# Kernel optimization log

Hardware: AMD Instinct MI355X
Metric: run time of the kernel (lower is better)

The kernel has to match this reference:

```python
import jax, jax.numpy as jnp
import numpy as np

B, N, D = 4, 4096, 128

def setup_inputs() -> dict:
    key = jax.random.key(0)
    k1, k2 = jax.random.split(key)
    x = jax.random.normal(k1, (B, N, D), dtype=jnp.float32)
    a = jax.random.normal(k2, (2 * D, 1), dtype=jnp.float32)
    return {"x": x, "a": a}

def reference(x, a):
    # matmul(cat([x_i, x_j], -1), a) == x_i @ a1 + x_j @ a2, so avoid the
    # O(B*N*N*2D) concat: compute two O(B*N) projections and broadcast-add.
    a1 = a[:D, 0]   # [D]
    a2 = a[D:, 0]   # [D]
    s_i = x @ a1    # [B, N]  (row / source term)
    s_j = x @ a2    # [B, N]  (col / target term)
    e = s_i[:, :, None] + s_j[:, None, :]          # [B, N, N]
    e = jnp.where(e > 0, e, 0.2 * e)               # leaky_relu(0.2)
    attention = jax.nn.softmax(e, axis=-1)         # row softmax
    return attention[..., None]                    # [B, N, N, 1]
```

## Files before the change

### kernel.cpp

```cpp
#include <hip/hip_runtime.h>

#define BB 4
#define NN 4096
#define DD 128
#define RB 8

__global__ __launch_bounds__(256) void score_kernel(const float* __restrict__ x,
                                                    const float* __restrict__ a,
                                                    float* __restrict__ si,
                                                    float* __restrict__ sj) {
    int wave = threadIdx.x >> 6;
    int lane = threadIdx.x & 63;
    int row  = blockIdx.x * 4 + wave;
    const float* xr = x + (size_t)row * DD;
    float x0 = xr[lane];
    float x1 = xr[lane + 64];
    float d1 = x0 * a[lane]      + x1 * a[lane + 64];
    float d2 = x0 * a[DD + lane] + x1 * a[DD + lane + 64];
    #pragma unroll
    for (int off = 32; off > 0; off >>= 1) {
        d1 += __shfl_down(d1, off, 64);
        d2 += __shfl_down(d2, off, 64);
    }
    if (lane == 0) {
        si[row] = d1;
        sj[row] = d2;
    }
}

__global__ __launch_bounds__(256) void softmax_kernel(const float* __restrict__ si_g,
                                                      const float* __restrict__ sj_g,
                                                      float* __restrict__ out) {
    __shared__ float red[4];

    const int bpb  = NN / RB;
    const int b    = blockIdx.x / bpb;
    const int i0   = (blockIdx.x % bpb) * RB;
    const int wave = threadIdx.x >> 6;
    const int lane = threadIdx.x & 63;

    const float* sjb = sj_g + b * NN;
    float4 sjv[16];
    float lmax = -INFINITY;
    #pragma unroll
    for (int g = 0; g < 16; ++g) {
        sjv[g] = *reinterpret_cast<const float4*>(sjb + g * 256 + lane * 4);
        lmax = fmaxf(fmaxf(fmaxf(sjv[g].x, sjv[g].y), fmaxf(sjv[g].z, sjv[g].w)), lmax);
    }
    #pragma unroll
    for (int off = 1; off < 64; off <<= 1)
        lmax = fmaxf(lmax, __shfl_xor(lmax, off, 64));
    if (lane == 0) red[wave] = lmax;
    __syncthreads();
    const float sjmax = fmaxf(fmaxf(red[0], red[1]), fmaxf(red[2], red[3]));

    #pragma unroll
    for (int r = 0; r < RB / 4; ++r) {
        const int i = i0 + wave * (RB / 4) + r;
        const float sival = si_g[b * NN + i];
        float m = sival + sjmax;
        m = m > 0.f ? m : 0.2f * m;

        float lsum = 0.f;
        #pragma unroll
        for (int g = 0; g < 16; ++g) {
            float e0 = sival + sjv[g].x; e0 = (e0 > 0.f ? e0 : 0.2f * e0) - m;
            float e1 = sival + sjv[g].y; e1 = (e1 > 0.f ? e1 : 0.2f * e1) - m;
            float e2 = sival + sjv[g].z; e2 = (e2 > 0.f ? e2 : 0.2f * e2) - m;
            float e3 = sival + sjv[g].w; e3 = (e3 > 0.f ? e3 : 0.2f * e3) - m;
            lsum += __expf(e0) + __expf(e1) + __expf(e2) + __expf(e3);
        }
        #pragma unroll
        for (int off = 1; off < 64; off <<= 1)
            lsum += __shfl_xor(lsum, off, 64);
        const float inv = 1.f / lsum;

        float* orow = out + (size_t)(b * NN + i) * NN;
        #pragma unroll
        for (int g = 0; g < 16; ++g) {
            float e0 = sival + sjv[g].x; e0 = (e0 > 0.f ? e0 : 0.2f * e0) - m;
            float e1 = sival + sjv[g].y; e1 = (e1 > 0.f ? e1 : 0.2f * e1) - m;
            float e2 = sival + sjv[g].z; e2 = (e2 > 0.f ? e2 : 0.2f * e2) - m;
            float e3 = sival + sjv[g].w; e3 = (e3 > 0.f ? e3 : 0.2f * e3) - m;
            float4 v = make_float4(__expf(e0) * inv, __expf(e1) * inv,
                                   __expf(e2) * inv, __expf(e3) * inv);
            *reinterpret_cast<float4*>(orow + g * 256 + lane * 4) = v;
        }
    }
}

extern "C" void kernel_launch(void* const* d_in, const int* in_sizes, int n_in,
                              void* d_out, int out_size, void* d_ws, size_t ws_size,
                              hipStream_t stream) {
    const float* x = (const float*)d_in[0];
    const float* a = (const float*)d_in[1];
    float* out = (float*)d_out;
    float* si = (float*)d_ws;
    float* sj = si + BB * NN;

    score_kernel<<<(BB * NN) / 4, 256, 0, stream>>>(x, a, si, sj);
    softmax_kernel<<<(BB * NN) / RB, 256, 0, stream>>>(si, sj, out);
}
```

Before: 52.62 us.

## Factor leaky-relu softmax exponentials into per-column precomputed exp terms

The score kernel now stores exp(s_j) and exp(0.2*s_j) per column instead of s_j. The softmax kernel rebuilds each element as a per-row scale times one of the two precomputed exponentials, choosing between them by comparing against exp(-s_i). This removes every per-element transcendental from both softmax passes. In exchange it doubles the per-column register footprint (32 float4), reads twice as much column data, and risks overflow or underflow of exp(s_j) for large scores, which changes numerical behaviour.

```diff
diff --git a/kernel.cpp b/kernel.cpp
--- a/kernel.cpp
+++ b/kernel.cpp
@@ -8,7 +8,7 @@
 __global__ __launch_bounds__(256) void score_kernel(const float* __restrict__ x,
                                                     const float* __restrict__ a,
                                                     float* __restrict__ si,
-                                                    float* __restrict__ sj) {
+                                                    float2* __restrict__ e12) {
     int wave = threadIdx.x >> 6;
     int lane = threadIdx.x & 63;
     int row  = blockIdx.x * 4 + wave;
@@ -18,72 +18,81 @@
     float d1 = x0 * a[lane]      + x1 * a[lane + 64];
     float d2 = x0 * a[DD + lane] + x1 * a[DD + lane + 64];
     #pragma unroll
-    for (int off = 32; off > 0; off >>= 1) {
-        d1 += __shfl_down(d1, off, 64);
-        d2 += __shfl_down(d2, off, 64);
+    for (int off = 1; off < 64; off <<= 1) {
+        d1 += __shfl_xor(d1, off, 64);
+        d2 += __shfl_xor(d2, off, 64);
     }
     if (lane == 0) {
         si[row] = d1;
-        sj[row] = d2;
+        e12[row] = make_float2(__expf(d2), __expf(0.2f * d2));
     }
 }
 
 __global__ __launch_bounds__(256) void softmax_kernel(const float* __restrict__ si_g,
-                                                      const float* __restrict__ sj_g,
+                                                      const float2* __restrict__ e12_g,
                                                       float* __restrict__ out) {
     __shared__ float red[4];
 
-    const int bpb  = NN / RB;
-    const int b    = blockIdx.x / bpb;
-    const int i0   = (blockIdx.x % bpb) * RB;
+    const int b    = blockIdx.x >> 9;
+    const int i0   = (blockIdx.x & 511) * RB;
     const int wave = threadIdx.x >> 6;
     const int lane = threadIdx.x & 63;
 
-    const float* sjb = sj_g + b * NN;
-    float4 sjv[16];
-    float lmax = -INFINITY;
+    const float* eb = (const float*)(e12_g + b * NN);
+    float4 ev[32];
+    float emax = 0.f;
     #pragma unroll
     for (int g = 0; g < 16; ++g) {
-        sjv[g] = *reinterpret_cast<const float4*>(sjb + g * 256 + lane * 4);
-        lmax = fmaxf(fmaxf(fmaxf(sjv[g].x, sjv[g].y), fmaxf(sjv[g].z, sjv[g].w)), lmax);
+        const float* p = eb + (size_t)(g * 256 + lane * 4) * 2;
+        ev[2 * g]     = *reinterpret_cast<const float4*>(p);
+        ev[2 * g + 1] = *reinterpret_cast<const float4*>(p + 4);
+        emax = fmaxf(emax, fmaxf(ev[2 * g].x,     ev[2 * g].z));
+        emax = fmaxf(emax, fmaxf(ev[2 * g + 1].x, ev[2 * g + 1].z));
     }
     #pragma unroll
     for (int off = 1; off < 64; off <<= 1)
-        lmax = fmaxf(lmax, __shfl_xor(lmax, off, 64));
-    if (lane == 0) red[wave] = lmax;
+        emax = fmaxf(emax, __shfl_xor(emax, off, 64));
+    if (lane == 0) red[wave] = emax;
     __syncthreads();
-    const float sjmax = fmaxf(fmaxf(red[0], red[1]), fmaxf(red[2], red[3]));
+    const float Emax = fmaxf(fmaxf(red[0], red[1]), fmaxf(red[2], red[3]));
+    const float mj = __logf(Emax);
 
     #pragma unroll
     for (int r = 0; r < RB / 4; ++r) {
         const int i = i0 + wave * (RB / 4) + r;
         const float sival = si_g[b * NN + i];
-        float m = sival + sjmax;
-        m = m > 0.f ? m : 0.2f * m;
+        const float c = sival + mj;
+        const float m = c > 0.f ? c : 0.2f * c;
+        const float T  = __expf(-sival);
+        const float A1 = __expf(sival - m);
+        const float A2 = __expf(0.2f * sival - m);
 
         float lsum = 0.f;
         #pragma unroll
         for (int g = 0; g < 16; ++g) {
-            float e0 = sival + sjv[g].x; e0 = (e0 > 0.f ? e0 : 0.2f * e0) - m;
-            float e1 = sival + sjv[g].y; e1 = (e1 > 0.f ? e1 : 0.2f * e1) - m;
-            float e2 = sival + sjv[g].z; e2 = (e2 > 0.f ? e2 : 0.2f * e2) - m;
-            float e3 = sival + sjv[g].w; e3 = (e3 > 0.f ? e3 : 0.2f * e3) - m;
-            lsum += __expf(e0) + __expf(e1) + __expf(e2) + __expf(e3);
+            float4 e0 = ev[2 * g], e1 = ev[2 * g + 1];
+            float p0 = (e0.x > T) ? A1 * e0.x : A2 * e0.y;
+            float p1 = (e0.z > T) ? A1 * e0.z : A2 * e0.w;
+            float p2 = (e1.x > T) ? A1 * e1.x : A2 * e1.y;
+            float p3 = (e1.z > T) ? A1 * e1.z : A2 * e1.w;
+            lsum += (p0 + p1) + (p2 + p3);
         }
         #pragma unroll
         for (int off = 1; off < 64; off <<= 1)
             lsum += __shfl_xor(lsum, off, 64);
         const float inv = 1.f / lsum;
+        const float B1 = A1 * inv;
+        const float B2 = A2 * inv;
 
         float* orow = out + (size_t)(b * NN + i) * NN;
         #pragma unroll
         for (int g = 0; g < 16; ++g) {
-            float e0 = sival + sjv[g].x; e0 = (e0 > 0.f ? e0 : 0.2f * e0) - m;
-            float e1 = sival + sjv[g].y; e1 = (e1 > 0.f ? e1 : 0.2f * e1) - m;
-            float e2 = sival + sjv[g].z; e2 = (e2 > 0.f ? e2 : 0.2f * e2) - m;
-            float e3 = sival + sjv[g].w; e3 = (e3 > 0.f ? e3 : 0.2f * e3) - m;
-            float4 v = make_float4(__expf(e0) * inv, __expf(e1) * inv,
-                                   __expf(e2) * inv, __expf(e3) * inv);
+            float4 e0 = ev[2 * g], e1 = ev[2 * g + 1];
+            float4 v;
+            v.x = (e0.x > T) ? B1 * e0.x : B2 * e0.y;
+            v.y = (e0.z > T) ? B1 * e0.z : B2 * e0.w;
+            v.z = (e1.x > T) ? B1 * e1.x : B2 * e1.y;
+            v.w = (e1.z > T) ? B1 * e1.z : B2 * e1.w;
             *reinterpret_cast<float4*>(orow + g * 256 + lane * 4) = v;
         }
     }
@@ -96,8 +105,8 @@
     const float* a = (const float*)d_in[1];
     float* out = (float*)d_out;
     float* si = (float*)d_ws;
-    float* sj = si + BB * NN;
+    float2* e12 = (float2*)(si + BB * NN);
 
-    score_kernel<<<(BB * NN) / 4, 256, 0, stream>>>(x, a, si, sj);
-    softmax_kernel<<<(BB * NN) / RB, 256, 0, stream>>>(si, sj, out);
+    score_kernel<<<(BB * NN) / 4, 256, 0, stream>>>(x, a, si, e12);
+    softmax_kernel<<<(BB * NN) / RB, 256, 0, stream>>>(si, e12, out);
 }
```

After: 64.78 us. 1.23x slower.
